# Performance work log

Hardware: AMD Instinct MI355X
Metric: run time of the kernel (lower is better)

Reference implementation:

```python
import jax, jax.numpy as jnp
import numpy as np

INPUT_DIM = 256
EMBED_DIM = 256
NUM_HEADS = 8
HEAD_DIM = EMBED_DIM // NUM_HEADS
N_TOKENS = 11136
N_BATCH = 16


def _xavier(key, shape):
    fan_out, fan_in = shape
    bound = np.sqrt(6.0 / (fan_in + fan_out)).astype(np.float32)
    return jax.random.uniform(key, shape, jnp.float32, -bound, bound)


def setup_inputs() -> dict:
    key = jax.random.key(0)
    k_x, k_ids, k_qkv, k_o = jax.random.split(key, 4)
    x = jax.random.normal(k_x, (N_TOKENS, INPUT_DIM), jnp.float32)
    batch_ids = jnp.sort(jax.random.randint(k_ids, (N_TOKENS,), 0, N_BATCH)).astype(jnp.int32)
    qkv_w = _xavier(k_qkv, (3 * EMBED_DIM, INPUT_DIM))
    qkv_b = jnp.zeros((3 * EMBED_DIM,), jnp.float32)
    o_w = _xavier(k_o, (EMBED_DIM, EMBED_DIM))
    o_b = jnp.zeros((EMBED_DIM,), jnp.float32)
    return {"x": x, "batch_ids": batch_ids, "qkv_w": qkv_w, "qkv_b": qkv_b,
            "o_w": o_w, "o_b": o_b}


def reference(x, batch_ids, qkv_w, qkv_b, o_w, o_b):
    # batch_ids is concrete metadata (mirrors np.unique on CPU in the original).
    ids = np.asarray(batch_ids)
    vals, counts = np.unique(ids, return_counts=True)
    B = len(vals)
    S = int(counts.max())
    offsets = np.concatenate([np.zeros(1, np.int64), np.cumsum(counts)[:-1]])
    seg = np.searchsorted(vals, ids)               # segment index per token
    pos = np.arange(ids.shape[0]) - offsets[seg]   # position within segment

    qkv = x @ qkv_w.T + qkv_b                      # [N, 3E]
    # pad_sequence with padding_value=1 -> scatter tokens into an all-ones buffer
    fin = jnp.ones((B, S, 3 * EMBED_DIM), qkv.dtype).at[seg, pos].set(qkv)
    # padded rows sum to exactly 3E (all ones) -> mask True marks padding
    pad_mask = fin.sum(-1) >= fin.shape[-1]        # [B, S]

    qkv4 = fin.reshape(B, S, NUM_HEADS, 3 * HEAD_DIM).transpose(0, 2, 1, 3)
    q, k, v = jnp.split(qkv4, 3, axis=-1)          # each [B, H, S, hd]

    logits = jnp.einsum('bhqd,bhkd->bhqk', q, k) * (HEAD_DIM ** -0.5)
    logits = jnp.where(pad_mask[:, None, None, :], -jnp.inf, logits)
    attn = jax.nn.softmax(logits, axis=-1)         # [B, H, S, S]

    out = jnp.einsum('bhqk,bhkd->bhqd', attn, v)
    out = out.transpose(0, 2, 1, 3).reshape(B, S, EMBED_DIM)
    out = out[seg, pos]                            # unpad -> [N, E]
    return out @ o_w.T + o_b
```

## Files before the change

### kernel.cpp

```cpp
#include <hip/hip_runtime.h>
#include <stdint.h>


#define N_TOK 11136
#define E 256
#define H 8
#define HD 32

typedef __attribute__((ext_vector_type(8))) __bf16 bf16x8;
typedef __attribute__((ext_vector_type(8))) unsigned short u16x8;
typedef __attribute__((ext_vector_type(4))) float f32x4;

__device__ __forceinline__ unsigned short f2bf(float f) {
  unsigned int u = __float_as_uint(f);
  u = (u + 0x7FFFu + ((u >> 16) & 1u)) >> 16;
  return (unsigned short)u;
}
__device__ __forceinline__ float bf2f(unsigned short s) {
  return __uint_as_float(((unsigned int)s) << 16);
}
__device__ __forceinline__ bf16x8 ld8(const unsigned short* p) {
  return *(const bf16x8*)p;
}
__device__ __forceinline__ unsigned int cvtpk(float a, float b) {
  unsigned int r;
  asm("v_cvt_pk_bf16_f32 %0, %1, %2" : "=v"(r) : "v"(a), "v"(b));
  return r;
}

__global__ void k_split(const float* __restrict__ x, const float* __restrict__ qw,
                        const float* __restrict__ ow, const int* __restrict__ ids,
                        unsigned short* __restrict__ xhi, unsigned short* __restrict__ xlo,
                        unsigned short* __restrict__ whi, unsigned short* __restrict__ wlo,
                        unsigned short* __restrict__ owb, int* __restrict__ offs) {
  if (blockIdx.x == 0 && threadIdx.x < 17) {
    int b = threadIdx.x, lo = 0, hi = N_TOK;
    while (lo < hi) { int mid = (lo + hi) >> 1; if (ids[mid] < b) lo = mid + 1; else hi = mid; }
    offs[b] = lo;
  }
  const int NX4 = N_TOK * E / 4;
  const int NW4 = 3 * E * E / 4;
  const int NO4 = E * E / 4;
  int total = NX4 + NW4 + NO4;
  for (int i = blockIdx.x * blockDim.x + threadIdx.x; i < total;
       i += gridDim.x * blockDim.x) {
    if (i < NX4) {
      float4 v = ((const float4*)x)[i];
      ushort4 hv, lv;
      hv.x = f2bf(v.x); lv.x = f2bf(v.x - bf2f(hv.x));
      hv.y = f2bf(v.y); lv.y = f2bf(v.y - bf2f(hv.y));
      hv.z = f2bf(v.z); lv.z = f2bf(v.z - bf2f(hv.z));
      hv.w = f2bf(v.w); lv.w = f2bf(v.w - bf2f(hv.w));
      ((ushort4*)xhi)[i] = hv; ((ushort4*)xlo)[i] = lv;
    } else if (i < NX4 + NW4) {
      int j = i - NX4;
      float4 v = ((const float4*)qw)[j];
      ushort4 hv, lv;
      hv.x = f2bf(v.x); lv.x = f2bf(v.x - bf2f(hv.x));
      hv.y = f2bf(v.y); lv.y = f2bf(v.y - bf2f(hv.y));
      hv.z = f2bf(v.z); lv.z = f2bf(v.z - bf2f(hv.z));
      hv.w = f2bf(v.w); lv.w = f2bf(v.w - bf2f(hv.w));
      ((ushort4*)whi)[j] = hv; ((ushort4*)wlo)[j] = lv;
    } else {
      int j = i - NX4 - NW4;
      float4 v = ((const float4*)ow)[j];
      ushort4 hv;
      hv.x = f2bf(v.x); hv.y = f2bf(v.y); hv.z = f2bf(v.z); hv.w = f2bf(v.w);
      ((ushort4*)owb)[j] = hv;
    }
  }
}

#define QK_BSTRIDE 264
#define QSCALE (0.17677669529663687f * 1.4426950408889634f)
__global__ __launch_bounds__(256, 3) void k_qkv(
    const unsigned short* __restrict__ xhi, const unsigned short* __restrict__ xlo,
    const unsigned short* __restrict__ whi, const unsigned short* __restrict__ wlo,
    const float* __restrict__ qkv_b,
    unsigned short* __restrict__ Qb, unsigned short* __restrict__ Kb,
    unsigned short* __restrict__ Vt) {
  int bid = blockIdx.x + 16 * blockIdx.y;
  int xcd = bid & 7;
  int j8 = bid >> 3;
  int colb = j8 & 15;
  int tile = (j8 >> 4) * 8 + xcd;
  if (tile >= 58) return;
  int col0 = colb * 48;
  __shared__ __align__(16) unsigned short Bhi[48 * QK_BSTRIDE];
  __shared__ __align__(16) unsigned short Blo[48 * QK_BSTRIDE];
  int tid = threadIdx.x;
  int w = tid >> 6, lane = tid & 63, m = lane & 15, quad = lane >> 4;
  int rowb = tile * 192 + w * 48;

  {
    const u16x8* wh8 = (const u16x8*)(whi + (size_t)col0 * E);
    const u16x8* wl8 = (const u16x8*)(wlo + (size_t)col0 * E);
#pragma unroll
    for (int i = 0; i < 6; ++i) {
      int flat = i * 256 + tid;
      int row = flat >> 5, c8 = flat & 31;
      *(u16x8*)(Bhi + row * QK_BSTRIDE + c8 * 8) = wh8[flat];
      *(u16x8*)(Blo + row * QK_BSTRIDE + c8 * 8) = wl8[flat];
    }
  }
  __syncthreads();

  f32x4 acc[3][3] = {};
  bf16x8 ah1[3], al1[3], ah2[3], al2[3];
#pragma unroll
  for (int mt = 0; mt < 3; ++mt) {
    const size_t ro = (size_t)(rowb + mt * 16 + m) * E + quad * 8;
    ah1[mt] = ld8(xhi + ro);       al1[mt] = ld8(xlo + ro);
    ah2[mt] = ld8(xhi + ro + 32);  al2[mt] = ld8(xlo + ro + 32);
  }
  for (int kc = 0; kc < 8; ++kc) {
    bf16x8 ah[3], al[3];
#pragma unroll
    for (int mt = 0; mt < 3; ++mt) {
      ah[mt] = ah1[mt]; al[mt] = al1[mt];
      ah1[mt] = ah2[mt]; al1[mt] = al2[mt];
    }
    int kn = kc + 2; if (kn > 7) kn = 7;
    int kon = kn * 32 + quad * 8;
#pragma unroll
    for (int mt = 0; mt < 3; ++mt) {
      const size_t ro = (size_t)(rowb + mt * 16 + m) * E + kon;
      ah2[mt] = ld8(xhi + ro);
      al2[mt] = ld8(xlo + ro);
    }
    int ko = kc * 32 + quad * 8;
#pragma unroll
    for (int t = 0; t < 3; ++t) {
      bf16x8 bh = ld8(Bhi + (16 * t + m) * QK_BSTRIDE + ko);
      bf16x8 bl = ld8(Blo + (16 * t + m) * QK_BSTRIDE + ko);
#pragma unroll
      for (int mt = 0; mt < 3; ++mt) {
        acc[mt][t] = __builtin_amdgcn_mfma_f32_16x16x32_bf16(ah[mt], bh, acc[mt][t], 0, 0, 0);
        acc[mt][t] = __builtin_amdgcn_mfma_f32_16x16x32_bf16(ah[mt], bl, acc[mt][t], 0, 0, 0);
        acc[mt][t] = __builtin_amdgcn_mfma_f32_16x16x32_bf16(al[mt], bh, acc[mt][t], 0, 0, 0);
      }
    }
  }
#pragma unroll
  for (int t = 0; t < 3; ++t) {
    int j = col0 + 16 * t + m;
    int hd = j / 96;
    int rr = j - hd * 96;
    float bias = qkv_b[j];
#pragma unroll
    for (int mt = 0; mt < 3; ++mt) {
      int tokb = rowb + mt * 16 + quad * 4;
      if (rr < 64) {
        float qsc = (rr < 32) ? QSCALE : 1.0f;
        unsigned short* dst = (rr < 32) ? (Qb + (size_t)hd * N_TOK * HD + rr)
                                        : (Kb + (size_t)hd * N_TOK * HD + (rr - 32));
#pragma unroll
        for (int r = 0; r < 4; ++r)
          dst[(size_t)(tokb + r) * HD] = f2bf((acc[mt][t][r] + bias) * qsc);
      } else {
        int d = rr - 64;
        ushort4 pk;
        pk.x = f2bf(acc[mt][t][0] + bias); pk.y = f2bf(acc[mt][t][1] + bias);
        pk.z = f2bf(acc[mt][t][2] + bias); pk.w = f2bf(acc[mt][t][3] + bias);
        *(ushort4*)(Vt + (size_t)(hd * HD + d) * N_TOK + tokb) = pk;
      }
    }
  }
}

#define PSTRIDE 72
#define VSTR 72
__global__ __launch_bounds__(256, 4) void k_attn(
    const int* __restrict__ ids, const int* __restrict__ offs,
    const unsigned short* __restrict__ Qb, const unsigned short* __restrict__ Kb,
    const unsigned short* __restrict__ Vt,
    unsigned short* __restrict__ attnb) {
  __shared__ __align__(16) unsigned short Kl[2][64 * 32];
  __shared__ __align__(16) unsigned short Vl[2][32 * VSTR];
  __shared__ __align__(16) unsigned short ldsP[4][16 * PSTRIDE];
  __shared__ int bred[8];
  int tid = threadIdx.x;
  int w = tid >> 6, lane = tid & 63;
  int m = lane & 15, quad = lane >> 4;
  int h = blockIdx.x;
  int tok0 = blockIdx.y * 64;
  int q0 = tok0 + w * 16;
  unsigned short* P = ldsP[w];
  int tok = q0 + m;
  int b = ids[tok];
  int st = offs[b], en = offs[b + 1];
  int kmin = st, kmax = en, stM = st, enm = en;
#pragma unroll
  for (int d = 1; d <= 8; d <<= 1) {
    kmin = min(kmin, __shfl_xor(kmin, d));
    kmax = max(kmax, __shfl_xor(kmax, d));
    stM  = max(stM,  __shfl_xor(stM,  d));
    enm  = min(enm,  __shfl_xor(enm,  d));
  }
  if (lane == 0) { bred[w] = kmin; bred[4 + w] = kmax; }
  __syncthreads();
  int kminB = min(min(bred[0], bred[1]), min(bred[2], bred[3]));
  int kmaxB = max(max(bred[4], bred[5]), max(bred[6], bred[7]));
  int k0beg = kminB & ~63;

  const unsigned short* Kbase = Kb + (size_t)h * N_TOK * HD;
  const unsigned short* Vbase = Vt + (size_t)h * HD * N_TOK;
  bf16x8 qf = ld8(Qb + (size_t)(h * N_TOK + tok) * HD + quad * 8);

  int krow = w * 16 + (lane >> 2);
  int kgof = (lane & 3) * 8;
  int vrow = w * 8 + (lane >> 3);
  int vgof = (lane & 7) * 8;

  bf16x8 kg = ld8(Kbase + (size_t)(k0beg + krow) * HD + kgof);
  bf16x8 vg = ld8(Vbase + (size_t)vrow * N_TOK + k0beg + vgof);
  *(bf16x8*)(&Kl[0][krow * 32 + kgof]) = kg;
  *(bf16x8*)(&Vl[0][vrow * VSTR + vgof]) = vg;
  __syncthreads();

  float lsum = 0.f;
  f32x4 o0 = {}, o1 = {};
  int buf = 0;
  for (int k0 = k0beg; k0 < kmaxB; k0 += 64) {
    int k1 = (k0 + 64 < kmaxB) ? (k0 + 64) : k0;
    kg = ld8(Kbase + (size_t)(k1 + krow) * HD + kgof);
    vg = ld8(Vbase + (size_t)vrow * N_TOK + k1 + vgof);
    const unsigned short* Kc = &Kl[buf][0];
    const unsigned short* Vc = &Vl[buf][0];
    f32x4 s[4];
    __builtin_amdgcn_s_setprio(1);
#pragma unroll
    for (int i = 0; i < 4; ++i) {
      bf16x8 kf = ld8(Kc + (16 * i + m) * 32 + quad * 8);
      f32x4 z = {};
      s[i] = __builtin_amdgcn_mfma_f32_16x16x32_bf16(kf, qf, z, 0, 0, 0);
    }
    __builtin_amdgcn_s_setprio(0);
    bool interior = (k0 >= stM && k0 + 64 <= enm);
    int jb = k0 + quad * 4;
#pragma unroll
    for (int i = 0; i < 4; ++i) {
      float p[4];
#pragma unroll
      for (int r = 0; r < 4; ++r) {
        float sv = s[i][r];
        if (!interior) {
          int j = jb + 16 * i + r;
          sv = (j >= st && j < en) ? sv : -3e38f;
        }
        float e;
        asm("v_exp_f32 %0, %1" : "=v"(e) : "v"(sv));
        p[r] = e;
      }
      lsum += (p[0] + p[1]) + (p[2] + p[3]);
      uint2 pk;
      pk.x = cvtpk(p[0], p[1]);
      pk.y = cvtpk(p[2], p[3]);
      *(uint2*)(P + m * PSTRIDE + 16 * i + quad * 4) = pk;
    }
    __builtin_amdgcn_s_setprio(1);
#pragma unroll
    for (int c = 0; c < 2; ++c) {
      bf16x8 pf  = ld8(P + m * PSTRIDE + 32 * c + quad * 8);
      bf16x8 vf0 = ld8(Vc + m * VSTR + 32 * c + quad * 8);
      bf16x8 vf1 = ld8(Vc + (16 + m) * VSTR + 32 * c + quad * 8);
      o0 = __builtin_amdgcn_mfma_f32_16x16x32_bf16(vf0, pf, o0, 0, 0, 0);
      o1 = __builtin_amdgcn_mfma_f32_16x16x32_bf16(vf1, pf, o1, 0, 0, 0);
    }
    __builtin_amdgcn_s_setprio(0);
    *(bf16x8*)(&Kl[buf ^ 1][krow * 32 + kgof]) = kg;
    *(bf16x8*)(&Vl[buf ^ 1][vrow * VSTR + vgof]) = vg;
    __syncthreads();
    buf ^= 1;
  }
  lsum += __shfl_xor(lsum, 16);
  lsum += __shfl_xor(lsum, 32);
  float inv = 1.0f / lsum;
  uint2 s0, s1;
  s0.x = cvtpk(o0[0] * inv, o0[1] * inv);
  s0.y = cvtpk(o0[2] * inv, o0[3] * inv);
  s1.x = cvtpk(o1[0] * inv, o1[1] * inv);
  s1.y = cvtpk(o1[2] * inv, o1[3] * inv);
  *(uint2*)(attnb + (size_t)tok * E + h * HD + quad * 4) = s0;
  *(uint2*)(attnb + (size_t)tok * E + h * HD + 16 + quad * 4) = s1;
}

__global__ __launch_bounds__(256, 4) void k_oproj(
    const unsigned short* __restrict__ attnb, const unsigned short* __restrict__ owb,
    const float* __restrict__ ob, float* __restrict__ out) {
  __shared__ __align__(16) unsigned short Bo[64 * QK_BSTRIDE];
  int tid = threadIdx.x;
  int w = tid >> 6, lane = tid & 63, m = lane & 15, quad = lane >> 4;
  int tok0 = blockIdx.x * 64, col0 = blockIdx.y * 64;
  {
    const u16x8* o8 = (const u16x8*)(owb + (size_t)col0 * E);
#pragma unroll
    for (int i = 0; i < 8; ++i) {
      int flat = i * 256 + tid;
      int row = flat >> 5, c8 = flat & 31;
      *(u16x8*)(Bo + row * QK_BSTRIDE + c8 * 8) = o8[flat];
    }
  }
  __syncthreads();
  f32x4 acc[4] = {};
  int arow = tok0 + 16 * w + m;
  const unsigned short* abase = attnb + (size_t)arow * E + quad * 8;
  bf16x8 a1 = ld8(abase);
  bf16x8 a2 = ld8(abase + 32);
  for (int kc = 0; kc < 8; ++kc) {
    bf16x8 a = a1;
    a1 = a2;
    int kn = kc + 2; if (kn > 7) kn = 7;
    a2 = ld8(abase + kn * 32);
    int ko = kc * 32 + quad * 8;
#pragma unroll
    for (int t = 0; t < 4; ++t) {
      bf16x8 b = ld8(Bo + (16 * t + m) * QK_BSTRIDE + ko);
      acc[t] = __builtin_amdgcn_mfma_f32_16x16x32_bf16(a, b, acc[t], 0, 0, 0);
    }
  }
#pragma unroll
  for (int t = 0; t < 4; ++t) {
    int j = col0 + 16 * t + m;
    float bias = ob[j];
#pragma unroll
    for (int r = 0; r < 4; ++r) {
      int tok = tok0 + 16 * w + quad * 4 + r;
      out[(size_t)tok * E + j] = acc[t][r] + bias;
    }
  }
}

extern "C" void kernel_launch(void* const* d_in, const int* in_sizes, int n_in,
                              void* d_out, int out_size, void* d_ws, size_t ws_size,
                              hipStream_t stream) {
  const float* x   = (const float*)d_in[0];
  const int*   ids = (const int*)d_in[1];
  const float* qw  = (const float*)d_in[2];
  const float* qb  = (const float*)d_in[3];
  const float* ow  = (const float*)d_in[4];
  const float* ob  = (const float*)d_in[5];
  float* out = (float*)d_out;

  char* p = (char*)d_ws;
  auto alloc = [&](size_t bytes) {
    char* r = p;
    p += (bytes + 255) & ~(size_t)255;
    return r;
  };
  int* offs = (int*)alloc(32 * sizeof(int));
  unsigned short* xhi = (unsigned short*)alloc((size_t)N_TOK * E * 2);
  unsigned short* xlo = (unsigned short*)alloc((size_t)N_TOK * E * 2);
  unsigned short* whi = (unsigned short*)alloc((size_t)3 * E * E * 2);
  unsigned short* wlo = (unsigned short*)alloc((size_t)3 * E * E * 2);
  unsigned short* owb = (unsigned short*)alloc((size_t)E * E * 2);
  unsigned short* Qb  = (unsigned short*)alloc((size_t)N_TOK * E * 2);
  unsigned short* Kb  = (unsigned short*)alloc((size_t)N_TOK * E * 2);
  unsigned short* Vt  = (unsigned short*)alloc((size_t)N_TOK * E * 2);
  unsigned short* att = (unsigned short*)alloc((size_t)N_TOK * E * 2);

  k_split<<<dim3(1712), dim3(256), 0, stream>>>(x, qw, ow, ids, xhi, xlo, whi, wlo, owb, offs);
  k_qkv<<<dim3(16, 64), dim3(256), 0, stream>>>(xhi, xlo, whi, wlo, qb, Qb, Kb, Vt);
  k_attn<<<dim3(H, N_TOK / 64), dim3(256), 0, stream>>>(ids, offs, Qb, Kb, Vt, att);
  k_oproj<<<dim3(N_TOK / 64, E / 64), dim3(256), 0, stream>>>(att, owb, ob, out);
}
```

Measured before the change: 151.9 us.

## Process two 16-query tiles per wave in attention kernel with 128-thread blocks

```diff
diff --git a/kernel.cpp b/kernel.cpp
--- a/kernel.cpp
+++ b/kernel.cpp
@@ -170,26 +170,29 @@
 
 #define PSTRIDE 72
 #define VSTR 72
-__global__ __launch_bounds__(256, 4) void k_attn(
+__global__ __launch_bounds__(128, 3) void k_attn(
     const int* __restrict__ ids, const int* __restrict__ offs,
     const unsigned short* __restrict__ Qb, const unsigned short* __restrict__ Kb,
     const unsigned short* __restrict__ Vt,
     unsigned short* __restrict__ attnb) {
   __shared__ __align__(16) unsigned short Kl[2][64 * 32];
   __shared__ __align__(16) unsigned short Vl[2][32 * VSTR];
-  __shared__ __align__(16) unsigned short ldsP[4][16 * PSTRIDE];
-  __shared__ int bred[8];
+  __shared__ __align__(16) unsigned short ldsP[2][32 * PSTRIDE];
+  __shared__ int bred[4];
   int tid = threadIdx.x;
   int w = tid >> 6, lane = tid & 63;
   int m = lane & 15, quad = lane >> 4;
   int h = blockIdx.x;
   int tok0 = blockIdx.y * 64;
-  int q0 = tok0 + w * 16;
+  int q0 = tok0 + w * 32;
   unsigned short* P = ldsP[w];
-  int tok = q0 + m;
-  int b = ids[tok];
-  int st = offs[b], en = offs[b + 1];
-  int kmin = st, kmax = en, stM = st, enm = en;
+  int tA = q0 + m;
+  int tB = q0 + 16 + m;
+  int bA = ids[tA], bB = ids[tB];
+  int st0 = offs[bA], en0 = offs[bA + 1];
+  int st1 = offs[bB], en1 = offs[bB + 1];
+  int kmin = min(st0, st1), kmax = max(en0, en1);
+  int stM = max(st0, st1), enm = min(en0, en1);
 #pragma unroll
   for (int d = 1; d <= 8; d <<= 1) {
     kmin = min(kmin, __shfl_xor(kmin, d));
@@ -197,92 +200,119 @@
     stM  = max(stM,  __shfl_xor(stM,  d));
     enm  = min(enm,  __shfl_xor(enm,  d));
   }
-  if (lane == 0) { bred[w] = kmin; bred[4 + w] = kmax; }
+  if (lane == 0) { bred[w] = kmin; bred[2 + w] = kmax; }
   __syncthreads();
-  int kminB = min(min(bred[0], bred[1]), min(bred[2], bred[3]));
-  int kmaxB = max(max(bred[4], bred[5]), max(bred[6], bred[7]));
+  int kminB = min(bred[0], bred[1]);
+  int kmaxB = max(bred[2], bred[3]);
   int k0beg = kminB & ~63;
 
   const unsigned short* Kbase = Kb + (size_t)h * N_TOK * HD;
   const unsigned short* Vbase = Vt + (size_t)h * HD * N_TOK;
-  bf16x8 qf = ld8(Qb + (size_t)(h * N_TOK + tok) * HD + quad * 8);
-
-  int krow = w * 16 + (lane >> 2);
-  int kgof = (lane & 3) * 8;
-  int vrow = w * 8 + (lane >> 3);
-  int vgof = (lane & 7) * 8;
-
-  bf16x8 kg = ld8(Kbase + (size_t)(k0beg + krow) * HD + kgof);
-  bf16x8 vg = ld8(Vbase + (size_t)vrow * N_TOK + k0beg + vgof);
-  *(bf16x8*)(&Kl[0][krow * 32 + kgof]) = kg;
-  *(bf16x8*)(&Vl[0][vrow * VSTR + vgof]) = vg;
+  bf16x8 qf0 = ld8(Qb + (size_t)(h * N_TOK + tA) * HD + quad * 8);
+  bf16x8 qf1 = ld8(Qb + (size_t)(h * N_TOK + tB) * HD + quad * 8);
+
+  int kr = tid >> 2;
+  int kgof = (tid & 3) * 8;
+  int vr = tid >> 3;
+  int vgof = (tid & 7) * 8;
+
+  bf16x8 kgA = ld8(Kbase + (size_t)(k0beg + kr) * HD + kgof);
+  bf16x8 kgB = ld8(Kbase + (size_t)(k0beg + 32 + kr) * HD + kgof);
+  bf16x8 vgA = ld8(Vbase + (size_t)vr * N_TOK + k0beg + vgof);
+  bf16x8 vgB = ld8(Vbase + (size_t)(16 + vr) * N_TOK + k0beg + vgof);
+  *(bf16x8*)(&Kl[0][kr * 32 + kgof]) = kgA;
+  *(bf16x8*)(&Kl[0][(32 + kr) * 32 + kgof]) = kgB;
+  *(bf16x8*)(&Vl[0][vr * VSTR + vgof]) = vgA;
+  *(bf16x8*)(&Vl[0][(16 + vr) * VSTR + vgof]) = vgB;
   __syncthreads();
 
-  float lsum = 0.f;
-  f32x4 o0 = {}, o1 = {};
+  float lsum0 = 0.f, lsum1 = 0.f;
+  f32x4 o00 = {}, o01 = {}, o10 = {}, o11 = {};
   int buf = 0;
   for (int k0 = k0beg; k0 < kmaxB; k0 += 64) {
     int k1 = (k0 + 64 < kmaxB) ? (k0 + 64) : k0;
-    kg = ld8(Kbase + (size_t)(k1 + krow) * HD + kgof);
-    vg = ld8(Vbase + (size_t)vrow * N_TOK + k1 + vgof);
+    kgA = ld8(Kbase + (size_t)(k1 + kr) * HD + kgof);
+    kgB = ld8(Kbase + (size_t)(k1 + 32 + kr) * HD + kgof);
+    vgA = ld8(Vbase + (size_t)vr * N_TOK + k1 + vgof);
+    vgB = ld8(Vbase + (size_t)(16 + vr) * N_TOK + k1 + vgof);
     const unsigned short* Kc = &Kl[buf][0];
     const unsigned short* Vc = &Vl[buf][0];
-    f32x4 s[4];
+    f32x4 s0[4], s1[4];
     __builtin_amdgcn_s_setprio(1);
 #pragma unroll
     for (int i = 0; i < 4; ++i) {
       bf16x8 kf = ld8(Kc + (16 * i + m) * 32 + quad * 8);
       f32x4 z = {};
-      s[i] = __builtin_amdgcn_mfma_f32_16x16x32_bf16(kf, qf, z, 0, 0, 0);
+      s0[i] = __builtin_amdgcn_mfma_f32_16x16x32_bf16(kf, qf0, z, 0, 0, 0);
+      f32x4 z2 = {};
+      s1[i] = __builtin_amdgcn_mfma_f32_16x16x32_bf16(kf, qf1, z2, 0, 0, 0);
     }
     __builtin_amdgcn_s_setprio(0);
     bool interior = (k0 >= stM && k0 + 64 <= enm);
     int jb = k0 + quad * 4;
 #pragma unroll
     for (int i = 0; i < 4; ++i) {
-      float p[4];
+      float p0[4], p1[4];
 #pragma unroll
       for (int r = 0; r < 4; ++r) {
-        float sv = s[i][r];
+        float sv0 = s0[i][r], sv1 = s1[i][r];
         if (!interior) {
           int j = jb + 16 * i + r;
-          sv = (j >= st && j < en) ? sv : -3e38f;
+          sv0 = (j >= st0 && j < en0) ? sv0 : -3e38f;
+          sv1 = (j >= st1 && j < en1) ? sv1 : -3e38f;
         }
-        float e;
-        asm("v_exp_f32 %0, %1" : "=v"(e) : "v"(sv));
-        p[r] = e;
+        float e0, e1;
+        asm("v_exp_f32 %0, %1" : "=v"(e0) : "v"(sv0));
+        asm("v_exp_f32 %0, %1" : "=v"(e1) : "v"(sv1));
+        p0[r] = e0; p1[r] = e1;
       }
-      lsum += (p[0] + p[1]) + (p[2] + p[3]);
-      uint2 pk;
-      pk.x = cvtpk(p[0], p[1]);
-      pk.y = cvtpk(p[2], p[3]);
-      *(uint2*)(P + m * PSTRIDE + 16 * i + quad * 4) = pk;
+      lsum0 += (p0[0] + p0[1]) + (p0[2] + p0[3]);
+      lsum1 += (p1[0] + p1[1]) + (p1[2] + p1[3]);
+      uint2 pk0, pk1;
+      pk0.x = cvtpk(p0[0], p0[1]); pk0.y = cvtpk(p0[2], p0[3]);
+      pk1.x = cvtpk(p1[0], p1[1]); pk1.y = cvtpk(p1[2], p1[3]);
+      *(uint2*)(P + m * PSTRIDE + 16 * i + quad * 4) = pk0;
+      *(uint2*)(P + (16 + m) * PSTRIDE + 16 * i + quad * 4) = pk1;
     }
     __builtin_amdgcn_s_setprio(1);
 #pragma unroll
     for (int c = 0; c < 2; ++c) {
-      bf16x8 pf  = ld8(P + m * PSTRIDE + 32 * c + quad * 8);
       bf16x8 vf0 = ld8(Vc + m * VSTR + 32 * c + quad * 8);
       bf16x8 vf1 = ld8(Vc + (16 + m) * VSTR + 32 * c + quad * 8);
-      o0 = __builtin_amdgcn_mfma_f32_16x16x32_bf16(vf0, pf, o0, 0, 0, 0);
-      o1 = __builtin_amdgcn_mfma_f32_16x16x32_bf16(vf1, pf, o1, 0, 0, 0);
+      bf16x8 pf0 = ld8(P + m * PSTRIDE + 32 * c + quad * 8);
+      bf16x8 pf1 = ld8(P + (16 + m) * PSTRIDE + 32 * c + quad * 8);
+      o00 = __builtin_amdgcn_mfma_f32_16x16x32_bf16(vf0, pf0, o00, 0, 0, 0);
+      o01 = __builtin_amdgcn_mfma_f32_16x16x32_bf16(vf1, pf0, o01, 0, 0, 0);
+      o10 = __builtin_amdgcn_mfma_f32_16x16x32_bf16(vf0, pf1, o10, 0, 0, 0);
+      o11 = __builtin_amdgcn_mfma_f32_16x16x32_bf16(vf1, pf1, o11, 0, 0, 0);
     }
     __builtin_amdgcn_s_setprio(0);
-    *(bf16x8*)(&Kl[buf ^ 1][krow * 32 + kgof]) = kg;
-    *(bf16x8*)(&Vl[buf ^ 1][vrow * VSTR + vgof]) = vg;
+    *(bf16x8*)(&Kl[buf ^ 1][kr * 32 + kgof]) = kgA;
+    *(bf16x8*)(&Kl[buf ^ 1][(32 + kr) * 32 + kgof]) = kgB;
+    *(bf16x8*)(&Vl[buf ^ 1][vr * VSTR + vgof]) = vgA;
+    *(bf16x8*)(&Vl[buf ^ 1][(16 + vr) * VSTR + vgof]) = vgB;
     __syncthreads();
     buf ^= 1;
   }
-  lsum += __shfl_xor(lsum, 16);
-  lsum += __shfl_xor(lsum, 32);
-  float inv = 1.0f / lsum;
-  uint2 s0, s1;
-  s0.x = cvtpk(o0[0] * inv, o0[1] * inv);
-  s0.y = cvtpk(o0[2] * inv, o0[3] * inv);
-  s1.x = cvtpk(o1[0] * inv, o1[1] * inv);
-  s1.y = cvtpk(o1[2] * inv, o1[3] * inv);
-  *(uint2*)(attnb + (size_t)tok * E + h * HD + quad * 4) = s0;
-  *(uint2*)(attnb + (size_t)tok * E + h * HD + 16 + quad * 4) = s1;
+  lsum0 += __shfl_xor(lsum0, 16);
+  lsum0 += __shfl_xor(lsum0, 32);
+  lsum1 += __shfl_xor(lsum1, 16);
+  lsum1 += __shfl_xor(lsum1, 32);
+  float inv0 = 1.0f / lsum0;
+  float inv1 = 1.0f / lsum1;
+  uint2 w00, w01, w10, w11;
+  w00.x = cvtpk(o00[0] * inv0, o00[1] * inv0);
+  w00.y = cvtpk(o00[2] * inv0, o00[3] * inv0);
+  w01.x = cvtpk(o01[0] * inv0, o01[1] * inv0);
+  w01.y = cvtpk(o01[2] * inv0, o01[3] * inv0);
+  w10.x = cvtpk(o10[0] * inv1, o10[1] * inv1);
+  w10.y = cvtpk(o10[2] * inv1, o10[3] * inv1);
+  w11.x = cvtpk(o11[0] * inv1, o11[1] * inv1);
+  w11.y = cvtpk(o11[2] * inv1, o11[3] * inv1);
+  *(uint2*)(attnb + (size_t)tA * E + h * HD + quad * 4) = w00;
+  *(uint2*)(attnb + (size_t)tA * E + h * HD + 16 + quad * 4) = w01;
+  *(uint2*)(attnb + (size_t)tB * E + h * HD + quad * 4) = w10;
+  *(uint2*)(attnb + (size_t)tB * E + h * HD + 16 + quad * 4) = w11;
 }
 
 __global__ __launch_bounds__(256, 4) void k_oproj(
@@ -361,6 +391,6 @@
 
   k_split<<<dim3(1712), dim3(256), 0, stream>>>(x, qw, ow, ids, xhi, xlo, whi, wlo, owb, offs);
   k_qkv<<<dim3(16, 64), dim3(256), 0, stream>>>(xhi, xlo, whi, wlo, qb, Qb, Kb, Vt);
-  k_attn<<<dim3(H, N_TOK / 64), dim3(256), 0, stream>>>(ids, offs, Qb, Kb, Vt, att);
+  k_attn<<<dim3(H, N_TOK / 64), dim3(128), 0, stream>>>(ids, offs, Qb, Kb, Vt, att);
   k_oproj<<<dim3(N_TOK / 64, E / 64), dim3(256), 0, stream>>>(att, owb, ob, out);
 }
```

Measured after the change: 157.5 us. 1.04x slower.

## Load K/V fragments directly into registers, dropping LDS staging and block barriers

Applied to the files above, without the earlier changes.

```diff
diff --git a/kernel.cpp b/kernel.cpp
--- a/kernel.cpp
+++ b/kernel.cpp
@@ -169,22 +169,17 @@
 }
 
 #define PSTRIDE 72
-#define VSTR 72
-__global__ __launch_bounds__(256, 4) void k_attn(
+__global__ __launch_bounds__(128, 4) void k_attn(
     const int* __restrict__ ids, const int* __restrict__ offs,
     const unsigned short* __restrict__ Qb, const unsigned short* __restrict__ Kb,
     const unsigned short* __restrict__ Vt,
     unsigned short* __restrict__ attnb) {
-  __shared__ __align__(16) unsigned short Kl[2][64 * 32];
-  __shared__ __align__(16) unsigned short Vl[2][32 * VSTR];
-  __shared__ __align__(16) unsigned short ldsP[4][16 * PSTRIDE];
-  __shared__ int bred[8];
+  __shared__ __align__(16) unsigned short ldsP[2][16 * PSTRIDE];
   int tid = threadIdx.x;
   int w = tid >> 6, lane = tid & 63;
   int m = lane & 15, quad = lane >> 4;
   int h = blockIdx.x;
-  int tok0 = blockIdx.y * 64;
-  int q0 = tok0 + w * 16;
+  int q0 = blockIdx.y * 32 + w * 16;
   unsigned short* P = ldsP[w];
   int tok = q0 + m;
   int b = ids[tok];
@@ -197,43 +192,47 @@
     stM  = max(stM,  __shfl_xor(stM,  d));
     enm  = min(enm,  __shfl_xor(enm,  d));
   }
-  if (lane == 0) { bred[w] = kmin; bred[4 + w] = kmax; }
-  __syncthreads();
-  int kminB = min(min(bred[0], bred[1]), min(bred[2], bred[3]));
-  int kmaxB = max(max(bred[4], bred[5]), max(bred[6], bred[7]));
-  int k0beg = kminB & ~63;
+  int k0beg = kmin & ~63;
 
   const unsigned short* Kbase = Kb + (size_t)h * N_TOK * HD;
   const unsigned short* Vbase = Vt + (size_t)h * HD * N_TOK;
   bf16x8 qf = ld8(Qb + (size_t)(h * N_TOK + tok) * HD + quad * 8);
 
-  int krow = w * 16 + (lane >> 2);
-  int kgof = (lane & 3) * 8;
-  int vrow = w * 8 + (lane >> 3);
-  int vgof = (lane & 7) * 8;
-
-  bf16x8 kg = ld8(Kbase + (size_t)(k0beg + krow) * HD + kgof);
-  bf16x8 vg = ld8(Vbase + (size_t)vrow * N_TOK + k0beg + vgof);
-  *(bf16x8*)(&Kl[0][krow * 32 + kgof]) = kg;
-  *(bf16x8*)(&Vl[0][vrow * VSTR + vgof]) = vg;
-  __syncthreads();
+  const unsigned short* Kp  = Kbase + (size_t)m * HD + quad * 8;
+  const unsigned short* Vp0 = Vbase + (size_t)m * N_TOK + quad * 8;
+  const unsigned short* Vp1 = Vbase + (size_t)(16 + m) * N_TOK + quad * 8;
+
+  bf16x8 kfn[4], vfn0[2], vfn1[2];
+#pragma unroll
+  for (int i = 0; i < 4; ++i) kfn[i] = ld8(Kp + (size_t)(k0beg + 16 * i) * HD);
+#pragma unroll
+  for (int c = 0; c < 2; ++c) {
+    vfn0[c] = ld8(Vp0 + k0beg + 32 * c);
+    vfn1[c] = ld8(Vp1 + k0beg + 32 * c);
+  }
 
   float lsum = 0.f;
   f32x4 o0 = {}, o1 = {};
-  int buf = 0;
-  for (int k0 = k0beg; k0 < kmaxB; k0 += 64) {
-    int k1 = (k0 + 64 < kmaxB) ? (k0 + 64) : k0;
-    kg = ld8(Kbase + (size_t)(k1 + krow) * HD + kgof);
-    vg = ld8(Vbase + (size_t)vrow * N_TOK + k1 + vgof);
-    const unsigned short* Kc = &Kl[buf][0];
-    const unsigned short* Vc = &Vl[buf][0];
+  for (int k0 = k0beg; k0 < kmax; k0 += 64) {
+    bf16x8 kf[4], vf0[2], vf1[2];
+#pragma unroll
+    for (int i = 0; i < 4; ++i) kf[i] = kfn[i];
+#pragma unroll
+    for (int c = 0; c < 2; ++c) { vf0[c] = vfn0[c]; vf1[c] = vfn1[c]; }
+    int k1 = (k0 + 64 < kmax) ? (k0 + 64) : k0;
+#pragma unroll
+    for (int i = 0; i < 4; ++i) kfn[i] = ld8(Kp + (size_t)(k1 + 16 * i) * HD);
+#pragma unroll
+    for (int c = 0; c < 2; ++c) {
+      vfn0[c] = ld8(Vp0 + k1 + 32 * c);
+      vfn1[c] = ld8(Vp1 + k1 + 32 * c);
+    }
     f32x4 s[4];
     __builtin_amdgcn_s_setprio(1);
 #pragma unroll
     for (int i = 0; i < 4; ++i) {
-      bf16x8 kf = ld8(Kc + (16 * i + m) * 32 + quad * 8);
       f32x4 z = {};
-      s[i] = __builtin_amdgcn_mfma_f32_16x16x32_bf16(kf, qf, z, 0, 0, 0);
+      s[i] = __builtin_amdgcn_mfma_f32_16x16x32_bf16(kf[i], qf, z, 0, 0, 0);
     }
     __builtin_amdgcn_s_setprio(0);
     bool interior = (k0 >= stM && k0 + 64 <= enm);
@@ -261,28 +260,22 @@
     __builtin_amdgcn_s_setprio(1);
 #pragma unroll
     for (int c = 0; c < 2; ++c) {
-      bf16x8 pf  = ld8(P + m * PSTRIDE + 32 * c + quad * 8);
-      bf16x8 vf0 = ld8(Vc + m * VSTR + 32 * c + quad * 8);
-      bf16x8 vf1 = ld8(Vc + (16 + m) * VSTR + 32 * c + quad * 8);
-      o0 = __builtin_amdgcn_mfma_f32_16x16x32_bf16(vf0, pf, o0, 0, 0, 0);
-      o1 = __builtin_amdgcn_mfma_f32_16x16x32_bf16(vf1, pf, o1, 0, 0, 0);
+      bf16x8 pf = ld8(P + m * PSTRIDE + 32 * c + quad * 8);
+      o0 = __builtin_amdgcn_mfma_f32_16x16x32_bf16(vf0[c], pf, o0, 0, 0, 0);
+      o1 = __builtin_amdgcn_mfma_f32_16x16x32_bf16(vf1[c], pf, o1, 0, 0, 0);
     }
     __builtin_amdgcn_s_setprio(0);
-    *(bf16x8*)(&Kl[buf ^ 1][krow * 32 + kgof]) = kg;
-    *(bf16x8*)(&Vl[buf ^ 1][vrow * VSTR + vgof]) = vg;
-    __syncthreads();
-    buf ^= 1;
   }
   lsum += __shfl_xor(lsum, 16);
   lsum += __shfl_xor(lsum, 32);
   float inv = 1.0f / lsum;
-  uint2 s0, s1;
-  s0.x = cvtpk(o0[0] * inv, o0[1] * inv);
-  s0.y = cvtpk(o0[2] * inv, o0[3] * inv);
-  s1.x = cvtpk(o1[0] * inv, o1[1] * inv);
-  s1.y = cvtpk(o1[2] * inv, o1[3] * inv);
-  *(uint2*)(attnb + (size_t)tok * E + h * HD + quad * 4) = s0;
-  *(uint2*)(attnb + (size_t)tok * E + h * HD + 16 + quad * 4) = s1;
+  uint2 w0, w1;
+  w0.x = cvtpk(o0[0] * inv, o0[1] * inv);
+  w0.y = cvtpk(o0[2] * inv, o0[3] * inv);
+  w1.x = cvtpk(o1[0] * inv, o1[1] * inv);
+  w1.y = cvtpk(o1[2] * inv, o1[3] * inv);
+  *(uint2*)(attnb + (size_t)tok * E + h * HD + quad * 4) = w0;
+  *(uint2*)(attnb + (size_t)tok * E + h * HD + 16 + quad * 4) = w1;
 }
 
 __global__ __launch_bounds__(256, 4) void k_oproj(
@@ -361,6 +354,6 @@
 
   k_split<<<dim3(1712), dim3(256), 0, stream>>>(x, qw, ow, ids, xhi, xlo, whi, wlo, owb, offs);
   k_qkv<<<dim3(16, 64), dim3(256), 0, stream>>>(xhi, xlo, whi, wlo, qb, Qb, Kb, Vt);
-  k_attn<<<dim3(H, N_TOK / 64), dim3(256), 0, stream>>>(ids, offs, Qb, Kb, Vt, att);
+  k_attn<<<dim3(H, N_TOK / 32), dim3(128), 0, stream>>>(ids, offs, Qb, Kb, Vt, att);
   k_oproj<<<dim3(N_TOK / 64, E / 64), dim3(256), 0, stream>>>(att, owb, ob, out);
 }
```

New measurement: 179.9 us. +18.4%, slower.
